# Kernel optimization log

Measured on AMD Instinct MI355X. Metric: run time of the kernel, lower is better.

## Reference

```python
import jax, jax.numpy as jnp
import numpy as np

DECAY = 0.99
EPS = 1e-5
NUM_EMBEDDINGS = 8192


def setup_inputs() -> dict:
    key = jax.random.key(0)
    k1, k2 = jax.random.split(key)
    N, D, K = 65536, 64, NUM_EMBEDDINGS
    x = jax.random.normal(k1, (N, D), dtype=jnp.float32)
    vq_embedding = jax.random.uniform(k2, (K, D), dtype=jnp.float32)
    vq_cluster_size = jnp.ones((K,), dtype=jnp.float32)
    return {"x": x, "vq_embedding": vq_embedding, "vq_cluster_size": vq_cluster_size}


def reference(x, vq_embedding, vq_cluster_size):
    N, D = x.shape
    K = vq_embedding.shape[0]

    # BatchNorm1d(affine=False), training mode: normalize with batch stats (biased var)
    mean = jnp.mean(x, axis=0)                      # [D]
    var = jnp.var(x, axis=0)                        # biased, [D]
    xn = (x - mean) / jnp.sqrt(var + EPS)           # [N, D]

    # pairwise squared distances [N, K]
    distances = (jnp.sum(xn * xn, axis=1, keepdims=True)
                 + jnp.sum(vq_embedding * vq_embedding, axis=1)
                 - 2.0 * (xn @ vq_embedding.T))
    idx = jnp.argmin(distances, axis=1)             # [N]

    # one-hot scatter expressed as segment sums
    dw = jax.ops.segment_sum(xn, idx, num_segments=K)                      # [K, D]
    counts = jax.ops.segment_sum(jnp.ones((N,), x.dtype), idx, num_segments=K)  # [K]

    # EMA codebook update
    new_emb = vq_cluster_size[:, None] * vq_embedding * DECAY + (1.0 - DECAY) * dw
    new_size = vq_cluster_size * DECAY + (1.0 - DECAY) * counts
    new_emb = new_emb / new_size[:, None]

    # BN running stats with momentum=None (cumulative avg, first batch):
    # running_mean = batch mean, running_var = unbiased batch var
    unbiased_var = var * (N / (N - 1))
    running_std = jnp.sqrt(unbiased_var + EPS)
    vq_embedding_output = new_emb * running_std[None, :] + mean[None, :]

    return vq_embedding_output, new_emb, new_size
```

## Files before the change

### kernel.cpp

```cpp
#include <hip/hip_runtime.h>

#define NROWS 65536
#define DIM 64
#define KCODES 8192
#define DECAYF 0.99f
#define EPSV 1e-5f
#define KD (KCODES * DIM)
#define KSPLIT 4
#define KC (KCODES / KSPLIT)
#define ROUNDS (KC / 128)

typedef _Float16 half8 __attribute__((ext_vector_type(8)));
typedef float f32x16 __attribute__((ext_vector_type(16)));

#define WS_STATS  0
#define WS_NHCK   256
#define WS_EBUF   8448
#define WS_PSUM   270592
#define WS_PSQ    286976
#define WS_PACKED 303360
#define WS_DW     434432
#define WS_COUNTS 958720

__global__ __launch_bounds__(256) void k_colstats_partial(
    const float* __restrict__ x, float* __restrict__ psum, float* __restrict__ psq)
{
    const int wave = threadIdx.x >> 6;
    const int col  = threadIdx.x & 63;
    const int base = blockIdx.x * 256;
    float s = 0.f, q = 0.f;
    #pragma unroll 4
    for (int i = 0; i < 64; ++i) {
        int r = base + i * 4 + wave;
        float v = x[(size_t)r * DIM + col];
        s += v;
        q += v * v;
    }
    __shared__ float ls[4][64];
    __shared__ float lq[4][64];
    ls[wave][col] = s;
    lq[wave][col] = q;
    __syncthreads();
    if (threadIdx.x < 64) {
        psum[blockIdx.x * 64 + col] = ls[0][col] + ls[1][col] + ls[2][col] + ls[3][col];
        psq[blockIdx.x * 64 + col]  = lq[0][col] + lq[1][col] + lq[2][col] + lq[3][col];
    }
}

__global__ void k_colstats_final(const float* __restrict__ psum,
                                 const float* __restrict__ psq,
                                 float* __restrict__ stats)
{
    const int col = threadIdx.x;
    float s = 0.f, q = 0.f;
    for (int i = 0; i < 256; ++i) {
        s += psum[i * 64 + col];
        q += psq[i * 64 + col];
    }
    const float n = (float)NROWS;
    float mean = s / n;
    float var = q / n - mean * mean;
    if (var < 0.f) var = 0.f;
    stats[col]       = mean;
    stats[64 + col]  = 1.0f / sqrtf(var + EPSV);
    stats[128 + col] = sqrtf(var * (n / (n - 1.0f)) + EPSV);
}

__global__ __launch_bounds__(256) void k_prep(const float* __restrict__ emb,
                                              half8* __restrict__ ebuf,
                                              float* __restrict__ nhck)
{
    const int tid = blockIdx.x * 256 + threadIdx.x;
    const int code = tid >> 3, sub = tid & 7;
    const int c = sub >> 1, h = sub & 1;
    const int d0 = c * 16 + h * 8;
    const float* e = emb + (size_t)code * DIM + d0;
    float4 a = *(const float4*)e;
    float4 b = *(const float4*)(e + 4);
    float f[8] = {a.x, a.y, a.z, a.w, b.x, b.y, b.z, b.w};
    half8 hh;
    float ssq = 0.f;
    #pragma unroll
    for (int i = 0; i < 8; ++i) {
        hh[i] = (_Float16)(f[i] - 0.5f);
        ssq += f[i] * f[i];
    }
    #pragma unroll
    for (int o = 1; o < 8; o <<= 1) ssq += __shfl_xor(ssq, o, 64);
    if (sub == 0) nhck[code] = -0.5f * ssq;
    const int R = code >> 7, t = (code >> 5) & 3, col = code & 31;
    ebuf[(size_t)R * 1024 + t * 256 + c * 64 + h * 32 + col] = hh;
}

__device__ __forceinline__ void gload16(const void* g, void* l)
{
    __builtin_amdgcn_global_load_lds(
        (const __attribute__((address_space(1))) void*)g,
        (__attribute__((address_space(3))) void*)l, 16, 0, 0);
}

__global__ __launch_bounds__(256, 4) void k_argmin32(
    const float* __restrict__ x, const half8* __restrict__ ebuf,
    const float* __restrict__ nhckg, const float* __restrict__ stats,
    unsigned long long* __restrict__ packed)
{
    __shared__ half8 smem[2048];

    const int lane = threadIdx.x & 63;
    const int wave = threadIdx.x >> 6;
    const int kc = blockIdx.y;
    const int col = lane & 31, h = lane >> 5;
    const int myrow = blockIdx.x * 128 + wave * 32 + col;

    half8 ah[4];
    {
        const float* xr = x + (size_t)myrow * DIM + h * 8;
        #pragma unroll
        for (int c = 0; c < 4; ++c) {
            float4 v0  = *(const float4*)(xr + c * 16);
            float4 v1  = *(const float4*)(xr + c * 16 + 4);
            float4 mu0 = *(const float4*)(stats + h * 8 + c * 16);
            float4 mu1 = *(const float4*)(stats + h * 8 + c * 16 + 4);
            float4 sg0 = *(const float4*)(stats + 64 + h * 8 + c * 16);
            float4 sg1 = *(const float4*)(stats + 64 + h * 8 + c * 16 + 4);
            ah[c][0] = (_Float16)((v0.x - mu0.x) * sg0.x);
            ah[c][1] = (_Float16)((v0.y - mu0.y) * sg0.y);
            ah[c][2] = (_Float16)((v0.z - mu0.z) * sg0.z);
            ah[c][3] = (_Float16)((v0.w - mu0.w) * sg0.w);
            ah[c][4] = (_Float16)((v1.x - mu1.x) * sg1.x);
            ah[c][5] = (_Float16)((v1.y - mu1.y) * sg1.y);
            ah[c][6] = (_Float16)((v1.z - mu1.z) * sg1.z);
            ah[c][7] = (_Float16)((v1.w - mu1.w) * sg1.w);
        }
    }

    float best[16];
    int bcode[16];
    #pragma unroll
    for (int i = 0; i < 16; ++i) { best[i] = -3.4e38f; bcode[i] = 0; }

    const half8* esrc = ebuf + (size_t)kc * (KC * 8);
    const float* ckb = nhckg + kc * KC;

    {
        const char* src = (const char*)esrc + threadIdx.x * 16;
        char* dst = (char*)smem + threadIdx.x * 16;
        #pragma unroll
        for (int i = 0; i < 4; ++i) gload16(src + i * 4096, dst + i * 4096);
    }
    float nhck[4];
    #pragma unroll
    for (int t = 0; t < 4; ++t) nhck[t] = ckb[t * 32 + col];
    __syncthreads();

    for (int R = 0; R < ROUNDS; ++R) {
        const int buf = R & 1;
        float nhck_n[4] = {0.f, 0.f, 0.f, 0.f};
        if (R < ROUNDS - 1) {
            const char* src = (const char*)esrc + (size_t)(R + 1) * 16384 + threadIdx.x * 16;
            char* dst = (char*)smem + (buf ^ 1) * 16384 + threadIdx.x * 16;
            #pragma unroll
            for (int i = 0; i < 4; ++i) gload16(src + i * 4096, dst + i * 4096);
            #pragma unroll
            for (int t = 0; t < 4; ++t) nhck_n[t] = ckb[(R + 1) * 128 + t * 32 + col];
        }

        const half8* sb = smem + buf * 1024 + lane;
        #pragma unroll
        for (int t = 0; t < 4; ++t) {
            half8 b0 = sb[t * 256];
            half8 b1 = sb[t * 256 + 64];
            half8 b2 = sb[t * 256 + 128];
            half8 b3 = sb[t * 256 + 192];
            f32x16 acc;
            #pragma unroll
            for (int i = 0; i < 16; ++i) acc[i] = nhck[t];
            __builtin_amdgcn_s_setprio(1);
            acc = __builtin_amdgcn_mfma_f32_32x32x16_f16(ah[0], b0, acc, 0, 0, 0);
            acc = __builtin_amdgcn_mfma_f32_32x32x16_f16(ah[1], b1, acc, 0, 0, 0);
            acc = __builtin_amdgcn_mfma_f32_32x32x16_f16(ah[2], b2, acc, 0, 0, 0);
            acc = __builtin_amdgcn_mfma_f32_32x32x16_f16(ah[3], b3, acc, 0, 0, 0);
            __builtin_amdgcn_s_setprio(0);
            const int codeb = R * 128 + t * 32 + col;
            #pragma unroll
            for (int i = 0; i < 16; ++i) {
                if (acc[i] > best[i]) { best[i] = acc[i]; bcode[i] = codeb; }
            }
        }
        __syncthreads();
        #pragma unroll
        for (int t = 0; t < 4; ++t) nhck[t] = nhck_n[t];
    }

    #pragma unroll
    for (int off = 1; off < 32; off <<= 1) {
        #pragma unroll
        for (int i = 0; i < 16; ++i) {
            float ow = __shfl_xor(best[i], off, 64);
            int oc = __shfl_xor(bcode[i], off, 64);
            if (ow > best[i] || (ow == best[i] && oc < bcode[i])) {
                best[i] = ow; bcode[i] = oc;
            }
        }
    }
    if (col == 0) {
        const int rbase = blockIdx.x * 128 + wave * 32 + 4 * h;
        #pragma unroll
        for (int i = 0; i < 16; ++i) {
            int row = rbase + (i & 3) + 8 * (i >> 2);
            unsigned u = __float_as_uint(best[i]);
            u = (u & 0x80000000u) ? ~u : (u | 0x80000000u);
            unsigned long long pk =
                ((unsigned long long)u << 32) |
                (unsigned)(8191 - (bcode[i] + kc * KC));
            atomicMax(&packed[row], pk);
        }
    }
}

__global__ __launch_bounds__(256) void k_scatter(
    const float* __restrict__ x, const float* __restrict__ stats,
    const unsigned long long* __restrict__ packed,
    float* __restrict__ dw, float* __restrict__ counts)
{
    const int t = blockIdx.x * 256 + threadIdx.x;
    const int row = t >> 6, col = t & 63;
    const int j = 8191 - (int)(packed[row] & 0xFFFFFFFFull);
    float xv = (x[(size_t)row * DIM + col] - stats[col]) * stats[64 + col];
    atomicAdd(&dw[(size_t)j * DIM + col], xv);
    if (col == 0) atomicAdd(&counts[j], 1.0f);
}

__global__ __launch_bounds__(256) void k_final(
    const float* __restrict__ emb, const float* __restrict__ cs,
    const float* __restrict__ dw, const float* __restrict__ counts,
    const float* __restrict__ stats, float* __restrict__ out)
{
    const int t = blockIdx.x * 256 + threadIdx.x;
    const int k = t >> 6, d = t & 63;
    float csk = cs[k];
    float ns = csk * DECAYF + (1.f - DECAYF) * counts[k];
    float ne = (csk * emb[t] * DECAYF + (1.f - DECAYF) * dw[t]) / ns;
    out[KD + t] = ne;
    out[t] = ne * stats[128 + d] + stats[d];
    if (d == 0) out[2 * KD + k] = ns;
}

extern "C" void kernel_launch(void* const* d_in, const int* in_sizes, int n_in,
                              void* d_out, int out_size, void* d_ws, size_t ws_size,
                              hipStream_t stream)
{
    const float* x   = (const float*)d_in[0];
    const float* emb = (const float*)d_in[1];
    const float* cs  = (const float*)d_in[2];
    float* out = (float*)d_out;
    float* ws  = (float*)d_ws;

    float* stats  = ws + WS_STATS;
    float* nhck   = ws + WS_NHCK;
    half8* ebuf   = (half8*)(ws + WS_EBUF);
    float* psum   = ws + WS_PSUM;
    float* psq    = ws + WS_PSQ;
    unsigned long long* packed = (unsigned long long*)(ws + WS_PACKED);
    float* dw     = ws + WS_DW;
    float* counts = ws + WS_COUNTS;

    hipMemsetAsync(ws + WS_PACKED, 0,
                   (size_t)(131072 + KD + KCODES) * sizeof(float), stream);

    k_colstats_partial<<<256, 256, 0, stream>>>(x, psum, psq);
    k_colstats_final<<<1, 64, 0, stream>>>(psum, psq, stats);
    k_prep<<<256, 256, 0, stream>>>(emb, ebuf, nhck);
    dim3 g3(NROWS / 128, KSPLIT);
    k_argmin32<<<g3, 256, 0, stream>>>(x, ebuf, nhck, stats, packed);
    k_scatter<<<(NROWS * DIM) / 256, 256, 0, stream>>>(x, stats, packed, dw, counts);
    k_final<<<KD / 256, 256, 0, stream>>>(emb, cs, dw, counts, stats, out);
}
```

Measured before the change: 172.6 us.

## Pack code index into low mantissa bits of score for single-fmax argmin

```diff
diff --git a/kernel.cpp b/kernel.cpp
--- a/kernel.cpp
+++ b/kernel.cpp
@@ -19,8 +19,8 @@
 #define WS_PSUM   270592
 #define WS_PSQ    286976
 #define WS_PACKED 303360
-#define WS_DW     434432
-#define WS_COUNTS 958720
+#define WS_DW     368896
+#define WS_COUNTS 893184
 
 __global__ __launch_bounds__(256) void k_colstats_partial(
     const float* __restrict__ x, float* __restrict__ psum, float* __restrict__ psq)
@@ -87,7 +87,7 @@
     }
     #pragma unroll
     for (int o = 1; o < 8; o <<= 1) ssq += __shfl_xor(ssq, o, 64);
-    if (sub == 0) nhck[code] = -0.5f * ssq;
+    if (sub == 0) nhck[code] = 10.6875f - 0.5f * ssq;
     const int R = code >> 7, t = (code >> 5) & 3, col = code & 31;
     ebuf[(size_t)R * 1024 + t * 256 + c * 64 + h * 32 + col] = hh;
 }
@@ -99,10 +99,10 @@
         (__attribute__((address_space(3))) void*)l, 16, 0, 0);
 }
 
-__global__ __launch_bounds__(256, 4) void k_argmin32(
+__global__ __launch_bounds__(256) void k_argmin32(
     const float* __restrict__ x, const half8* __restrict__ ebuf,
     const float* __restrict__ nhckg, const float* __restrict__ stats,
-    unsigned long long* __restrict__ packed)
+    unsigned* __restrict__ packed)
 {
     __shared__ half8 smem[2048];
 
@@ -135,9 +135,8 @@
     }
 
     float best[16];
-    int bcode[16];
-    #pragma unroll
-    for (int i = 0; i < 16; ++i) { best[i] = -3.4e38f; bcode[i] = 0; }
+    #pragma unroll
+    for (int i = 0; i < 16; ++i) best[i] = -3.4e38f;
 
     const half8* esrc = ebuf + (size_t)kc * (KC * 8);
     const float* ckb = nhckg + kc * KC;
@@ -181,10 +180,11 @@
             acc = __builtin_amdgcn_mfma_f32_32x32x16_f16(ah[2], b2, acc, 0, 0, 0);
             acc = __builtin_amdgcn_mfma_f32_32x32x16_f16(ah[3], b3, acc, 0, 0, 0);
             __builtin_amdgcn_s_setprio(0);
-            const int codeb = R * 128 + t * 32 + col;
+            const unsigned key = (unsigned)(8191 - (kc * KC + R * 128 + t * 32 + col));
             #pragma unroll
             for (int i = 0; i < 16; ++i) {
-                if (acc[i] > best[i]) { best[i] = acc[i]; bcode[i] = codeb; }
+                unsigned u = (__float_as_uint(acc[i]) & 0xFFFFE000u) | key;
+                best[i] = fmaxf(best[i], __uint_as_float(u));
             }
         }
         __syncthreads();
@@ -195,13 +195,8 @@
     #pragma unroll
     for (int off = 1; off < 32; off <<= 1) {
         #pragma unroll
-        for (int i = 0; i < 16; ++i) {
-            float ow = __shfl_xor(best[i], off, 64);
-            int oc = __shfl_xor(bcode[i], off, 64);
-            if (ow > best[i] || (ow == best[i] && oc < bcode[i])) {
-                best[i] = ow; bcode[i] = oc;
-            }
-        }
+        for (int i = 0; i < 16; ++i)
+            best[i] = fmaxf(best[i], __shfl_xor(best[i], off, 64));
     }
     if (col == 0) {
         const int rbase = blockIdx.x * 128 + wave * 32 + 4 * h;
@@ -210,22 +205,21 @@
             int row = rbase + (i & 3) + 8 * (i >> 2);
             unsigned u = __float_as_uint(best[i]);
             u = (u & 0x80000000u) ? ~u : (u | 0x80000000u);
-            unsigned long long pk =
-                ((unsigned long long)u << 32) |
-                (unsigned)(8191 - (bcode[i] + kc * KC));
-            atomicMax(&packed[row], pk);
+            atomicMax(&packed[row], u);
         }
     }
 }
 
 __global__ __launch_bounds__(256) void k_scatter(
     const float* __restrict__ x, const float* __restrict__ stats,
-    const unsigned long long* __restrict__ packed,
+    const unsigned* __restrict__ packed,
     float* __restrict__ dw, float* __restrict__ counts)
 {
     const int t = blockIdx.x * 256 + threadIdx.x;
     const int row = t >> 6, col = t & 63;
-    const int j = 8191 - (int)(packed[row] & 0xFFFFFFFFull);
+    const unsigned v = packed[row];
+    const unsigned key = (v & 0x80000000u) ? (v & 8191u) : (~v & 8191u);
+    const int j = 8191 - (int)key;
     float xv = (x[(size_t)row * DIM + col] - stats[col]) * stats[64 + col];
     atomicAdd(&dw[(size_t)j * DIM + col], xv);
     if (col == 0) atomicAdd(&counts[j], 1.0f);
@@ -261,12 +255,12 @@
     half8* ebuf   = (half8*)(ws + WS_EBUF);
     float* psum   = ws + WS_PSUM;
     float* psq    = ws + WS_PSQ;
-    unsigned long long* packed = (unsigned long long*)(ws + WS_PACKED);
+    unsigned* packed = (unsigned*)(ws + WS_PACKED);
     float* dw     = ws + WS_DW;
     float* counts = ws + WS_COUNTS;
 
     hipMemsetAsync(ws + WS_PACKED, 0,
-                   (size_t)(131072 + KD + KCODES) * sizeof(float), stream);
+                   (size_t)(65536 + KD + KCODES) * sizeof(float), stream);
 
     k_colstats_partial<<<256, 256, 0, stream>>>(x, psum, psq);
     k_colstats_final<<<1, 64, 0, stream>>>(psum, psq, stats);
```

Result: faster. 157.9 us (-8.5%).
